# Optimization experiments

Hardware: AMD Instinct MI355X
Metric: run time of the kernel (lower is better)

The kernel has to match this reference:

```python
import jax, jax.numpy as jnp
import numpy as np

# Config constants (repo-level globals)
N, S, P = 4096, 64, 64          # total peds, scenes, peds per scene (uniform)
H, E, MLPD, BOT = 64, 16, 64, 32  # h_dim, EMBEDDING_DIM, MLP_DIM, BOTTLENECK_DIM
PRED_LEN = 12
MIN_DIM = 3                      # mlp_input_dim = [rel_pos(2), speed(1)]
PP_HID = 512                     # hidden width of mlp_pre_pool


def setup_inputs() -> dict:
    key = jax.random.key(0)
    ks = jax.random.split(key, 24)
    sc = 0.1
    starts = jnp.arange(S, dtype=jnp.int32) * P
    inp = {
        "last_pos": jax.random.normal(ks[0], (N, 2), jnp.float32),
        "last_pos_rel": jax.random.normal(ks[1], (N, 2), jnp.float32),
        "h0": jax.random.normal(ks[2], (1, N, H), jnp.float32),
        "c0": jax.random.normal(ks[3], (1, N, H), jnp.float32),
        "pred_ped_speed": jax.random.uniform(ks[4], (PRED_LEN, N, 1), jnp.float32),
        # spatial_embedding: Linear(3, E)
        "W_sp": jax.random.normal(ks[5], (MIN_DIM, E)) * sc, "b_sp": jnp.zeros(E),
        # LSTM cell (torch gate order i,f,g,o)
        "W_ih": jax.random.normal(ks[6], (E, 4 * H)) * sc, "b_ih": jnp.zeros(4 * H),
        "W_hh": jax.random.normal(ks[7], (H, 4 * H)) * sc, "b_hh": jnp.zeros(4 * H),
        # hidden2pos: Linear(H, 2)
        "W_h2p": jax.random.normal(ks[8], (H, 2)) * sc, "b_h2p": jnp.zeros(2),
        # pooling pos_embedding: Linear(3, E)
        "W_pe": jax.random.normal(ks[9], (MIN_DIM, E)) * sc, "b_pe": jnp.zeros(E),
        # mlp_pre_pool: [E+H, 512, BOT], relu, no BN
        "W_pp1": jax.random.normal(ks[10], (E + H, PP_HID)) * sc, "b_pp1": jnp.zeros(PP_HID),
        "W_pp2": jax.random.normal(ks[11], (PP_HID, BOT)) * sc, "b_pp2": jnp.zeros(BOT),
        # decoder mlp: [H+BOT, MLPD, H], relu, no BN
        "W_m1": jax.random.normal(ks[12], (H + BOT, MLPD)) * sc, "b_m1": jnp.zeros(MLPD),
        "W_m2": jax.random.normal(ks[13], (MLPD, H)) * sc, "b_m2": jnp.zeros(H),
        "seq_start_end": jnp.stack([starts, starts + P], axis=1),
        "train_or_test": 0,
    }
    return inp


def reference(last_pos, last_pos_rel, h0, c0, pred_ped_speed,
              W_sp, b_sp, W_ih, b_ih, W_hh, b_hh, W_h2p, b_h2p,
              W_pe, b_pe, W_pp1, b_pp1, W_pp2, b_pp2,
              W_m1, b_m1, W_m2, b_m2, seq_start_end, train_or_test):
    relu = jax.nn.relu

    def lstm_cell(x, h, c):
        g = x @ W_ih + b_ih + h @ W_hh + b_hh
        i, f, gg, o = jnp.split(g, 4, axis=-1)
        c = jax.nn.sigmoid(f) * c + jax.nn.sigmoid(i) * jnp.tanh(gg)
        h = jax.nn.sigmoid(o) * jnp.tanh(c)
        return h, c

    def pool(h, pos, spd):
        # uniform scenes: reshape [N,*] -> [S,P,*]; pairwise index [s,i,j]
        hg = h.reshape(S, P, H)
        pg = pos.reshape(S, P, 2)
        sg = spd.reshape(S, P, 1)
        # social feature [s,i,j] = pos[j] - pos[i]  (curr_end_pos_1 - curr_end_pos_2)
        rel = pg[:, None, :, :] - pg[:, :, None, :]              # [S,P,P,2]
        feat = jnp.concatenate(
            [rel, jnp.broadcast_to(sg[:, None, :, :], (S, P, P, 1))], -1)  # speed of j
        emb = feat @ W_pe + b_pe                                  # [S,P,P,E]
        pre = jnp.concatenate(
            [jnp.broadcast_to(hg[:, None, :, :], (S, P, P, H)), emb], -1)  # h of j
        x = relu(pre @ W_pp1 + b_pp1)
        x = relu(x @ W_pp2 + b_pp2)                               # [S,P,P,BOT]
        return x.max(axis=2).reshape(-1, BOT)                     # max over j -> [N,BOT]

    # speed used at step id is pred_ped_speed[id+1], last step reuses final speed
    spd_seq = jnp.concatenate([pred_ped_speed[1:], pred_ped_speed[-1:]], axis=0)
    x0 = jnp.concatenate([last_pos_rel, pred_ped_speed[0]], -1) @ W_sp + b_sp

    def step(carry, spd_t):
        h, c, lp, x = carry
        h, c = lstm_cell(x, h, c)
        rel_pos = h @ W_h2p + b_h2p
        curr = rel_pos + lp
        x_new = jnp.concatenate([rel_pos, spd_t], -1) @ W_sp + b_sp
        pool_h = pool(h, curr, spd_t)
        h_new = relu(relu(jnp.concatenate([h, pool_h], -1) @ W_m1 + b_m1) @ W_m2 + b_m2)
        return (h_new, c, curr, x_new), rel_pos

    carry = (h0[0], c0[0], last_pos, x0)
    _, rels = jax.lax.scan(step, carry, spd_seq)
    return rels  # [PRED_LEN, N, 2]
```

## Files before the change

kernel.cpp:

```cpp
#include <hip/hip_runtime.h>

typedef unsigned int  u32;
typedef unsigned short u16;
typedef float  f32x4 __attribute__((ext_vector_type(4)));
typedef u32    u32x4 __attribute__((ext_vector_type(4)));
typedef __bf16 bf16x8 __attribute__((ext_vector_type(8)));
typedef _Float16 f16;
typedef _Float16 f16x8 __attribute__((ext_vector_type(8)));
typedef _Float16 f16x2 __attribute__((ext_vector_type(2)));

static constexpr int NPED = 4096;
static constexpr int H = 64, E = 16, BOT = 32, PPH = 512;
static constexpr int TSTEPS = 12;

__device__ __forceinline__ float bf2f(u16 u) {
  return __builtin_bit_cast(float, ((u32)u) << 16);
}
__device__ __forceinline__ u16 f2bf(float f) {
  u32 u = __builtin_bit_cast(u32, f);
  u += 0x7fffu + ((u >> 16) & 1u);
  return (u16)(u >> 16);
}
__device__ __forceinline__ u16 f2h(float f) {
  return __builtin_bit_cast(u16, (f16)f);
}
__device__ __forceinline__ float sigm(float x) { return 1.f / (1.f + __expf(-x)); }
__device__ __forceinline__ float tanhf_(float x) {
  float t = fabsf(x);
  float e = __expf(-2.f * t);
  float r = (1.f - e) / (1.f + e);
  return x < 0.f ? -r : r;
}
__device__ __forceinline__ f16x8 relu8(f16x8 t) {
  const f16x8 z = {(f16)0, (f16)0, (f16)0, (f16)0, (f16)0, (f16)0, (f16)0, (f16)0};
#if __has_builtin(__builtin_elementwise_max)
  return __builtin_elementwise_max(t, z);
#else
  #pragma unroll
  for (int q = 0; q < 8; ++q) t[q] = t[q] > (f16)0 ? t[q] : (f16)0;
  return t;
#endif
}

static constexpr size_t OFF_C    = 0;
static constexpr size_t OFF_HL   = 1048576;
static constexpr size_t OFF_POS  = 2097152;
static constexpr size_t OFF_X    = 2129920;
static constexpr size_t OFF_POOL = 2392064;
static constexpr size_t OFF_ABF  = 2916352;
static constexpr size_t OFF_A3   = 7110656;
static constexpr size_t OFF_CST  = 7116800;
static constexpr size_t OFF_W2T  = 7118848;
static constexpr size_t OFF_GWH  = 7151616;
static constexpr size_t OFF_GWL  = 7200768;
static constexpr size_t OFF_D1H  = 7249920;
static constexpr size_t OFF_D1L  = 7262208;
static constexpr size_t OFF_D2H  = 7274496;
static constexpr size_t OFF_D2L  = 7282688;
static constexpr size_t OFF_PWH  = 7290880;
static constexpr size_t OFF_PWL  = 7356416;
static constexpr size_t OFF_ABF2 = 7421952;
static constexpr size_t ABF_BYTES = (size_t)NPED * PPH * 2;
static constexpr size_t WS_NEED_FUSED = OFF_ABF2 + ABF_BYTES;

static constexpr int POOL_SMEM = 64*520*2 + 32*520*2 + 16*512*2 + 16*4*2*16*4;
static constexpr int FUSED_SMEM = POOL_SMEM + 64 + 128 + 128;

__global__ void k_setup(const float* __restrict__ last_pos, const float* __restrict__ last_pos_rel,
                        const float* __restrict__ c0, const float* __restrict__ pps,
                        const float* __restrict__ W_sp, const float* __restrict__ b_sp,
                        const float* __restrict__ W_pe, const float* __restrict__ b_pe,
                        const float* __restrict__ W_pp1, const float* __restrict__ b_pp1,
                        const float* __restrict__ W_pp2,
                        const float* __restrict__ W_ih, const float* __restrict__ W_hh,
                        const float* __restrict__ W_m1, const float* __restrict__ W_m2,
                        float* __restrict__ c, float* __restrict__ pos, float* __restrict__ x,
                        float* __restrict__ A3, float* __restrict__ Cst, u16* __restrict__ W2t,
                        u16* GWH, u16* GWL, u16* D1H, u16* D1L,
                        u16* D2H, u16* D2L, u16* PWH, u16* PWL)
{
  const int stride = gridDim.x * blockDim.x;
  const int tid0 = blockIdx.x * blockDim.x + threadIdx.x;
  for (int i = tid0; i < NPED * H; i += stride) c[i] = c0[i];
  for (int i = tid0; i < NPED * 2; i += stride) pos[i] = last_pos[i];
  for (int i = tid0; i < NPED * E; i += stride) {
    int n = i >> 4, e = i & 15;
    x[i] = last_pos_rel[2*n] * W_sp[e] + last_pos_rel[2*n+1] * W_sp[16+e]
         + pps[n] * W_sp[32+e] + b_sp[e];
  }
  for (int i = tid0; i < 3 * PPH; i += stride) {
    int r = i >> 9, k = i & 511;
    float s = 0.f;
    for (int e = 0; e < 16; ++e) s += W_pe[r*16+e] * W_pp1[(64+e)*PPH + k];
    A3[i] = s;
  }
  for (int i = tid0; i < PPH; i += stride) {
    float s = b_pp1[i];
    for (int e = 0; e < 16; ++e) s += b_pe[e] * W_pp1[(64+e)*PPH + i];
    Cst[i] = s;
  }
  for (int i = tid0; i < 32 * PPH; i += stride) {
    int n = i >> 9, k = i & 511;
    W2t[i] = f2h(W_pp2[k*32 + n]);
  }
  for (int i = tid0; i < 256*96; i += stride) {
    int n = i / 96, k = i - n*96;
    float wv = (k < 16) ? W_ih[k*256+n] : ((k < 80) ? W_hh[(k-16)*256+n] : 0.f);
    u16 hi = f2bf(wv); u16 lo = f2bf(wv - bf2f(hi));
    int idx = (((n>>4)*3 + (k>>5))*64 + ((k>>3)&3)*16 + (n&15))*8 + (k&7);
    GWH[idx] = hi; GWL[idx] = lo;
  }
  for (int i = tid0; i < 64*96; i += stride) {
    int n = i / 96, k = i - n*96;
    float wv = W_m1[k*64 + n];
    u16 hi = f2bf(wv); u16 lo = f2bf(wv - bf2f(hi));
    int idx = (((n>>4)*3 + (k>>5))*64 + ((k>>3)&3)*16 + (n&15))*8 + (k&7);
    D1H[idx] = hi; D1L[idx] = lo;
  }
  for (int i = tid0; i < 64*64; i += stride) {
    int n = i >> 6, k = i & 63;
    float wv = W_m2[k*64 + n];
    u16 hi = f2bf(wv); u16 lo = f2bf(wv - bf2f(hi));
    int idx = (((n>>4)*2 + (k>>5))*64 + ((k>>3)&3)*16 + (n&15))*8 + (k&7);
    D2H[idx] = hi; D2L[idx] = lo;
  }
  for (int i = tid0; i < 512*64; i += stride) {
    int n = i >> 6, k = i & 63;
    float wv = W_pp1[k*PPH + n];
    u16 hi = f2bf(wv); u16 lo = f2bf(wv - bf2f(hi));
    int idx = (((n>>4)*2 + (k>>5))*64 + ((k>>3)&3)*16 + (n&15))*8 + (k&7);
    PWH[idx] = hi; PWL[idx] = lo;
  }
}

template<int NT, int NKS>
__device__ __forceinline__ void load_frags(const u16* __restrict__ WH, const u16* __restrict__ WL,
                                           int tile0, int lane,
                                           u32x4 (&bh)[NT][NKS], u32x4 (&bl)[NT][NKS])
{
  #pragma unroll
  for (int i = 0; i < NT; ++i)
    #pragma unroll
    for (int ks = 0; ks < NKS; ++ks) {
      int o = (((tile0 + i)*NKS + ks)*64 + lane)*8;
      bh[i][ks] = *(const u32x4*)(WH + o);
      bl[i][ks] = *(const u32x4*)(WL + o);
    }
}

template<int NT, int NKS>
__device__ __forceinline__ void mfma_compute(const u32x4 (&bh)[NT][NKS], const u32x4 (&bl)[NT][NKS],
                                             int lane, const float* arow, f32x4* acc)
{
  const int kg = lane >> 4;
  #pragma unroll
  for (int ks = 0; ks < NKS; ++ks) {
    f32x4 a0 = *(const f32x4*)(arow + ks*32 + kg*8);
    f32x4 a1 = *(const f32x4*)(arow + ks*32 + kg*8 + 4);
    float av[8] = {a0.x,a0.y,a0.z,a0.w,a1.x,a1.y,a1.z,a1.w};
    bf16x8 ah, al;
    #pragma unroll
    for (int j = 0; j < 8; ++j) {
      __bf16 hbits = (__bf16)av[j];
      ah[j] = hbits;
      al[j] = (__bf16)(av[j] - (float)hbits);
    }
    #pragma unroll
    for (int i = 0; i < NT; ++i) {
      bf16x8 BH = __builtin_bit_cast(bf16x8, bh[i][ks]);
      bf16x8 BL = __builtin_bit_cast(bf16x8, bl[i][ks]);
      acc[i] = __builtin_amdgcn_mfma_f32_16x16x32_bf16(ah, BH, acc[i], 0, 0, 0);
      acc[i] = __builtin_amdgcn_mfma_f32_16x16x32_bf16(ah, BL, acc[i], 0, 0, 0);
      acc[i] = __builtin_amdgcn_mfma_f32_16x16x32_bf16(al, BH, acc[i], 0, 0, 0);
    }
  }
}

template<int NT, int NKS>
__device__ __forceinline__ void mfma_block(
    const u16* __restrict__ WH, const u16* __restrict__ WL, int tile0, int lane,
    const float* arow, int acol0, f32x4* acc)
{
  u32x4 bh[NT][NKS], bl[NT][NKS];
  load_frags<NT,NKS>(WH, WL, tile0, lane, bh, bl);
  mfma_compute<NT,NKS>(bh, bl, lane, arow + acol0, acc);
}

__global__ __launch_bounds__(256) void k_step(
    int t,
    const float* __restrict__ h0, const float* __restrict__ pps,
    float* __restrict__ c, float* __restrict__ h_lstm,
    float* __restrict__ pos, float* __restrict__ x, const float* __restrict__ pool,
    const float* __restrict__ b_ih, const float* __restrict__ b_hh,
    const float* __restrict__ W_h2p, const float* __restrict__ b_h2p,
    const float* __restrict__ W_sp, const float* __restrict__ b_sp,
    const float* __restrict__ b_m1, const float* __restrict__ b_m2,
    const float* __restrict__ A3, const float* __restrict__ Cst,
    const u16* __restrict__ GWH, const u16* __restrict__ GWL,
    const u16* __restrict__ D1H, const u16* __restrict__ D1L,
    const u16* __restrict__ D2H, const u16* __restrict__ D2L,
    const u16* __restrict__ PWH, const u16* __restrict__ PWL,
    u16* __restrict__ a_bf, float* __restrict__ out)
{
  __shared__ float zin[16][100];
  __shared__ float o1[16][68];
  __shared__ float as_[16][100];
  __shared__ float hl[16][68];
  __shared__ float gl[16][260];
  __shared__ float rel_s[16][2], pos_s[16][2], spd_s[16];

  const int tid = threadIdx.x;
  const int p0 = blockIdx.x * 16;
  const int w = tid >> 6, lane = tid & 63, colq = lane & 15, kg = lane >> 4;
  const int tsp = (t + 1 < 12) ? t + 1 : 11;

  { int p = tid >> 4, e = tid & 15;
    as_[p][e] = x[(p0 + p) * E + e];
    as_[p][80 + e] = 0.f; }
  if (tid < 16) spd_s[tid] = pps[tsp * NPED + p0 + tid];
  if (t == 0) {
    #pragma unroll
    for (int q = 0; q < 4; ++q) {
      int idx = tid + 256*q; int p = idx >> 6, d = idx & 63;
      as_[p][16 + d] = h0[(p0 + p) * H + d];
    }
  } else {
    #pragma unroll
    for (int q = 0; q < 4; ++q) {
      int idx = tid + 256*q; int p = idx >> 6, d = idx & 63;
      zin[p][d] = h_lstm[(p0 + p) * H + d];
    }
    #pragma unroll
    for (int q = 0; q < 2; ++q) {
      int idx = tid + 256*q; int p = idx >> 5, d = idx & 31;
      zin[p][64 + d] = pool[(p0 + p) * BOT + d];
    }
  }
  __syncthreads();

  if (t > 0) {
    {
      f32x4 acc = {0.f, 0.f, 0.f, 0.f};
      mfma_block<1,3>(D1H, D1L, w, lane, &zin[colq][0], 0, &acc);
      int n = w*16 + colq;
      float bm = b_m1[n];
      #pragma unroll
      for (int r = 0; r < 4; ++r) o1[kg*4 + r][n] = fmaxf(acc[r] + bm, 0.f);
    }
    __syncthreads();
    {
      f32x4 acc = {0.f, 0.f, 0.f, 0.f};
      mfma_block<1,2>(D2H, D2L, w, lane, &o1[colq][0], 0, &acc);
      int n = w*16 + colq;
      float bm = b_m2[n];
      #pragma unroll
      for (int r = 0; r < 4; ++r) as_[kg*4 + r][16 + n] = fmaxf(acc[r] + bm, 0.f);
    }
    __syncthreads();
  }

  {
    f32x4 gacc[4];
    #pragma unroll
    for (int i = 0; i < 4; ++i) gacc[i] = (f32x4){0.f,0.f,0.f,0.f};
    mfma_block<2,3>(GWH, GWL, w*4,     lane, &as_[colq][0], 0, &gacc[0]);
    mfma_block<2,3>(GWH, GWL, w*4 + 2, lane, &as_[colq][0], 0, &gacc[2]);
    #pragma unroll
    for (int i = 0; i < 4; ++i) {
      int n = (w*4 + i)*16 + colq;
      float bb = b_ih[n] + b_hh[n];
      #pragma unroll
      for (int r = 0; r < 4; ++r) gl[kg*4 + r][n] = gacc[i][r] + bb;
    }
  }
  __syncthreads();

  #pragma unroll
  for (int q = 0; q < 4; ++q) {
    int idx = tid + 256*q; int p = idx >> 6, d = idx & 63; int n = p0 + p;
    float gi = gl[p][d], gf = gl[p][64 + d], gg = gl[p][128 + d], go = gl[p][192 + d];
    float cv = c[n*H + d];
    float cn = sigm(gf) * cv + sigm(gi) * tanhf_(gg);
    float hv = sigm(go) * tanhf_(cn);
    c[n*H + d] = cn;
    hl[p][d] = hv;
    h_lstm[n*H + d] = hv;
  }
  __syncthreads();

  {
    int p = tid >> 4, l = tid & 15;
    f32x4 hv = *(const f32x4*)(&hl[p][0] + l*4);
    float s0 = hv.x * W_h2p[(l*4+0)*2]   + hv.y * W_h2p[(l*4+1)*2]
             + hv.z * W_h2p[(l*4+2)*2]   + hv.w * W_h2p[(l*4+3)*2];
    float s1 = hv.x * W_h2p[(l*4+0)*2+1] + hv.y * W_h2p[(l*4+1)*2+1]
             + hv.z * W_h2p[(l*4+2)*2+1] + hv.w * W_h2p[(l*4+3)*2+1];
    #pragma unroll
    for (int m = 1; m < 16; m <<= 1) {
      s0 += __shfl_xor(s0, m, 64);
      s1 += __shfl_xor(s1, m, 64);
    }
    if (l == 0) {
      float r0 = s0 + b_h2p[0], r1 = s1 + b_h2p[1];
      int n = p0 + p;
      float px = pos[n*2] + r0, py = pos[n*2+1] + r1;
      pos[n*2] = px; pos[n*2+1] = py;
      rel_s[p][0] = r0; rel_s[p][1] = r1;
      pos_s[p][0] = px; pos_s[p][1] = py;
      out[(t*NPED + n)*2] = r0; out[(t*NPED + n)*2 + 1] = r1;
    }
  }
  __syncthreads();

  if (t < 11) {
    {
      int p = tid >> 4, e = tid & 15;
      float xv = rel_s[p][0] * W_sp[e] + rel_s[p][1] * W_sp[16+e]
               + spd_s[p] * W_sp[32+e] + b_sp[e];
      x[(p0 + p) * E + e] = xv;
    }
    {
      f32x4 pacc[8];
      #pragma unroll
      for (int i = 0; i < 8; ++i) pacc[i] = (f32x4){0.f,0.f,0.f,0.f};
      mfma_block<4,2>(PWH, PWL, w*8,     lane, &hl[colq][0], 0, &pacc[0]);
      mfma_block<4,2>(PWH, PWL, w*8 + 4, lane, &hl[colq][0], 0, &pacc[4]);
      #pragma unroll
      for (int i = 0; i < 8; ++i) {
        int n = (w*8 + i)*16 + colq;
        float a3x = A3[n], a3y = A3[512 + n], a3s = A3[1024 + n], cst = Cst[n];
        #pragma unroll
        for (int r = 0; r < 4; ++r) {
          int p2 = kg*4 + r;
          float val = pacc[i][r] + pos_s[p2][0]*a3x + pos_s[p2][1]*a3y
                    + spd_s[p2]*a3s + cst;
          a_bf[(size_t)(p0 + p2)*PPH + n] = f2h(val);
        }
      }
    }
  }
}

__global__ __launch_bounds__(1024) void k_pool(
    const u16* __restrict__ a_bf, const float* __restrict__ pos,
    const float* __restrict__ A3, const u16* __restrict__ W2t,
    const float* __restrict__ b_pp2, float* __restrict__ pool)
{
  constexpr int LDA = 520;
  extern __shared__ char smem_raw[];
  u16* a_s  = (u16*)smem_raw;
  u16* w2_s = a_s + 64 * LDA;
  f16* v_s  = (f16*)(w2_s + 32 * LDA);
  float* red = (float*)(v_s + 16 * 512);

  const int tid = threadIdx.x;
  const int s = blockIdx.y;
  const int i0 = blockIdx.x * 16;

  for (int idx = tid; idx < 4096; idx += 1024) {
    int r = idx >> 6, c8 = (idx & 63) * 8;
    *(u32x4*)&a_s[r * LDA + c8] = *(const u32x4*)&a_bf[(s * 64 + r) * PPH + c8];
  }
  for (int idx = tid; idx < 2048; idx += 1024) {
    int r = idx >> 6, c8 = (idx & 63) * 8;
    *(u32x4*)&w2_s[r * LDA + c8] = *(const u32x4*)&W2t[r * PPH + c8];
  }
  for (int idx = tid; idx < 4096; idx += 1024) {
    int i = idx >> 8, k2 = (idx & 255) * 2;
    int n = s * 64 + i0 + i;
    float px = pos[n * 2], py = pos[n * 2 + 1];
    float v0 = px * A3[k2]     + py * A3[512 + k2];
    float v1 = px * A3[k2 + 1] + py * A3[512 + k2 + 1];
    f16x2 pk = { (f16)v0, (f16)v1 };
    *(f16x2*)&v_s[i * 512 + k2] = pk;
  }
  __syncthreads();

  const int lane = tid & 63, w = tid >> 6;
  const int jq = w & 3, g = w >> 2;
  const int col = lane & 15, kg = lane >> 4;
  const int aoff  = (jq * 16 + col) * LDA + kg * 8;
  const int w0off = col * LDA + kg * 8;
  const int w1off = (col + 16) * LDA + kg * 8;
  const float b20 = b_pp2[col];
  const float b21 = b_pp2[col + 16];
  const f32x4 vzero = {0.f, 0.f, 0.f, 0.f};

  f32x4 accA[4], accB[4];
  #pragma unroll
  for (int ii = 0; ii < 4; ++ii) { accA[ii] = vzero; accB[ii] = vzero; }

  for (int kk = 0; kk < 16; ++kk) {
    const int ke = kk * 32;
    f16x8 a8  = __builtin_bit_cast(f16x8, *(const u32x4*)&a_s[aoff + ke]);
    f16x8 bw0 = __builtin_bit_cast(f16x8, *(const u32x4*)&w2_s[w0off + ke]);
    f16x8 bw1 = __builtin_bit_cast(f16x8, *(const u32x4*)&w2_s[w1off + ke]);
    #pragma unroll
    for (int ii = 0; ii < 4; ++ii) {
      f16x8 v8 = *(const f16x8*)&v_s[(g * 4 + ii) * 512 + ke + kg * 8];
      f16x8 tq = relu8(a8 - v8);
      accA[ii] = __builtin_amdgcn_mfma_f32_16x16x32_f16(tq, bw0, accA[ii], 0, 0, 0);
      accB[ii] = __builtin_amdgcn_mfma_f32_16x16x32_f16(tq, bw1, accB[ii], 0, 0, 0);
    }
  }

  #pragma unroll
  for (int ii = 0; ii < 4; ++ii) {
    float m0 = 0.f, m1 = 0.f;
    #pragma unroll
    for (int r = 0; r < 4; ++r) {
      m0 = fmaxf(m0, accA[ii][r] + b20);
      m1 = fmaxf(m1, accB[ii][r] + b21);
    }
    m0 = fmaxf(m0, __shfl_xor(m0, 16, 64));
    m0 = fmaxf(m0, __shfl_xor(m0, 32, 64));
    m1 = fmaxf(m1, __shfl_xor(m1, 16, 64));
    m1 = fmaxf(m1, __shfl_xor(m1, 32, 64));
    if (kg == 0) {
      red[((w * 4 + ii) * 2 + 0) * 16 + col] = m0;
      red[((w * 4 + ii) * 2 + 1) * 16 + col] = m1;
    }
  }
  __syncthreads();

  if (tid < 512) {
    int gg = tid >> 7, ii = (tid >> 5) & 3, tile = (tid >> 4) & 1, cc = tid & 15;
    float m = red[(((gg * 4 + 0) * 4 + ii) * 2 + tile) * 16 + cc];
    #pragma unroll
    for (int q = 1; q < 4; ++q)
      m = fmaxf(m, red[(((gg * 4 + q) * 4 + ii) * 2 + tile) * 16 + cc]);
    int i = i0 + gg * 4 + ii;
    pool[(s * 64 + i) * 32 + tile * 16 + cc] = m;
  }
}

__global__ __launch_bounds__(1024) void k_fused(
    int t,
    const float* __restrict__ pps,
    float* __restrict__ c, float* __restrict__ h_lstm,
    float* __restrict__ pos, float* __restrict__ x,
    const float* __restrict__ b_ih, const float* __restrict__ b_hh,
    const float* __restrict__ W_h2p, const float* __restrict__ b_h2p,
    const float* __restrict__ W_sp, const float* __restrict__ b_sp,
    const float* __restrict__ b_m1, const float* __restrict__ b_m2,
    const float* __restrict__ A3, const float* __restrict__ Cst,
    const u16* __restrict__ GWH, const u16* __restrict__ GWL,
    const u16* __restrict__ D1H, const u16* __restrict__ D1L,
    const u16* __restrict__ D2H, const u16* __restrict__ D2L,
    const u16* __restrict__ PWH, const u16* __restrict__ PWL,
    const u16* __restrict__ W2t, const float* __restrict__ b_pp2,
    const u16* __restrict__ a_read, u16* __restrict__ a_write,
    float* __restrict__ out)
{
  constexpr int LDA = 520;
  extern __shared__ char smem_raw[];
  u16*   a_s    = (u16*)smem_raw;
  u16*   w2_s   = a_s + 64 * LDA;
  f16*   v_s    = (f16*)(w2_s + 32 * LDA);
  float* red    = (float*)(v_s + 16 * 512);
  float* spd_s  = red + 16*4*2*16;
  float* rel_s  = spd_s + 16;
  float* pos_s  = rel_s + 32;
  float* zin = (float*)smem_raw;
  float* o1  = zin + 16*100;
  float* as_ = o1  + 16*68;
  float* hl  = as_ + 16*100;
  float* gl  = hl  + 16*68;

  const int tid = threadIdx.x;
  const int s = blockIdx.y;
  const int i0 = blockIdx.x * 16;
  const int p0 = s * 64 + i0;
  const int lane = tid & 63, w = tid >> 6;
  const int colq = lane & 15, kg = lane >> 4;
  const int sd = tid & 63;
  const int tsp = (t + 1 < 12) ? t + 1 : 11;

  float hreg = h_lstm[(p0 + w) * H + sd];
  float creg = c[(p0 + w) * H + sd];
  float whp0 = W_h2p[2 * sd], whp1 = W_h2p[2 * sd + 1];
  float xreg = 0.f;
  if (tid < 256) xreg = x[(p0 + (tid >> 4)) * E + (tid & 15)];
  if (tid < 16) spd_s[tid] = pps[tsp * NPED + p0 + tid];

  for (int idx = tid; idx < 4096; idx += 1024) {
    int r = idx >> 6, c8 = (idx & 63) * 8;
    *(u32x4*)&a_s[r * LDA + c8] = *(const u32x4*)&a_read[(s * 64 + r) * PPH + c8];
  }
  for (int idx = tid; idx < 2048; idx += 1024) {
    int r = idx >> 6, c8 = (idx & 63) * 8;
    *(u32x4*)&w2_s[r * LDA + c8] = *(const u32x4*)&W2t[r * PPH + c8];
  }
  for (int idx = tid; idx < 4096; idx += 1024) {
    int i = idx >> 8, k2 = (idx & 255) * 2;
    int n = s * 64 + i0 + i;
    float px = pos[n * 2], py = pos[n * 2 + 1];
    float v0 = px * A3[k2]     + py * A3[512 + k2];
    float v1 = px * A3[k2 + 1] + py * A3[512 + k2 + 1];
    f16x2 pk = { (f16)v0, (f16)v1 };
    *(f16x2*)&v_s[i * 512 + k2] = pk;
  }
  __syncthreads();

  u32x4 gh[1][3], glo[1][3];
  u32x4 d1h_[1][3], d1l_[1][3], d2h_[1][2], d2l_[1][2];

  {
    const int jq = w & 3, g = w >> 2;
    const int aoff  = (jq * 16 + colq) * LDA + kg * 8;
    const int w0off = colq * LDA + kg * 8;
    const int w1off = (colq + 16) * LDA + kg * 8;
    const float b20 = b_pp2[colq];
    const float b21 = b_pp2[colq + 16];
    const f32x4 vzero = {0.f, 0.f, 0.f, 0.f};

    f32x4 accA[4], accB[4];
    #pragma unroll
    for (int ii = 0; ii < 4; ++ii) { accA[ii] = vzero; accB[ii] = vzero; }

    for (int kk = 0; kk < 16; ++kk) {
      const int ke = kk * 32;
      f16x8 a8  = __builtin_bit_cast(f16x8, *(const u32x4*)&a_s[aoff + ke]);
      f16x8 bw0 = __builtin_bit_cast(f16x8, *(const u32x4*)&w2_s[w0off + ke]);
      f16x8 bw1 = __builtin_bit_cast(f16x8, *(const u32x4*)&w2_s[w1off + ke]);
      #pragma unroll
      for (int ii = 0; ii < 4; ++ii) {
        f16x8 v8 = *(const f16x8*)&v_s[(g * 4 + ii) * 512 + ke + kg * 8];
        f16x8 tq = relu8(a8 - v8);
        accA[ii] = __builtin_amdgcn_mfma_f32_16x16x32_f16(tq, bw0, accA[ii], 0, 0, 0);
        accB[ii] = __builtin_amdgcn_mfma_f32_16x16x32_f16(tq, bw1, accB[ii], 0, 0, 0);
      }
    }

    #pragma unroll
    for (int ii = 0; ii < 4; ++ii) {
      float m0 = 0.f, m1 = 0.f;
      #pragma unroll
      for (int r = 0; r < 4; ++r) {
        m0 = fmaxf(m0, accA[ii][r] + b20);
        m1 = fmaxf(m1, accB[ii][r] + b21);
      }
      m0 = fmaxf(m0, __shfl_xor(m0, 16, 64));
      m0 = fmaxf(m0, __shfl_xor(m0, 32, 64));
      m1 = fmaxf(m1, __shfl_xor(m1, 16, 64));
      m1 = fmaxf(m1, __shfl_xor(m1, 32, 64));
      if (kg == 0) {
        red[((w * 4 + ii) * 2 + 0) * 16 + colq] = m0;
        red[((w * 4 + ii) * 2 + 1) * 16 + colq] = m1;
      }
    }
  }
  load_frags<1,3>(GWH, GWL, w, lane, gh, glo);
  if (w < 4) {
    load_frags<1,3>(D1H, D1L, w, lane, d1h_, d1l_);
    load_frags<1,2>(D2H, D2L, w, lane, d2h_, d2l_);
  }
  __syncthreads();

  zin[w * 100 + sd] = hreg;
  if (tid < 512) {
    int gg = tid >> 7, ii = (tid >> 5) & 3, tile = (tid >> 4) & 1, cc = tid & 15;
    float m = red[(((gg * 4 + 0) * 4 + ii) * 2 + tile) * 16 + cc];
    #pragma unroll
    for (int q = 1; q < 4; ++q)
      m = fmaxf(m, red[(((gg * 4 + q) * 4 + ii) * 2 + tile) * 16 + cc]);
    zin[(gg * 4 + ii) * 100 + 64 + tile * 16 + cc] = m;
  }
  if (tid < 256) { int p = tid >> 4, e = tid & 15;
                   as_[p * 100 + e] = xreg; as_[p * 100 + 80 + e] = 0.f; }
  __syncthreads();

  if (w < 4) {
    f32x4 acc = {0.f, 0.f, 0.f, 0.f};
    mfma_compute<1,3>(d1h_, d1l_, lane, &zin[colq * 100], &acc);
    int n = w * 16 + colq;
    float bm = b_m1[n];
    #pragma unroll
    for (int r = 0; r < 4; ++r) o1[(kg * 4 + r) * 68 + n] = fmaxf(acc[r] + bm, 0.f);
  }
  __syncthreads();

  if (w < 4) {
    f32x4 acc = {0.f, 0.f, 0.f, 0.f};
    mfma_compute<1,2>(d2h_, d2l_, lane, &o1[colq * 68], &acc);
    int n = w * 16 + colq;
    float bm = b_m2[n];
    #pragma unroll
    for (int r = 0; r < 4; ++r) as_[(kg * 4 + r) * 100 + 16 + n] = fmaxf(acc[r] + bm, 0.f);
  }
  __syncthreads();

  {
    f32x4 acc = {0.f, 0.f, 0.f, 0.f};
    mfma_compute<1,3>(gh, glo, lane, &as_[colq * 100], &acc);
    int n = w * 16 + colq;
    float bb = b_ih[n] + b_hh[n];
    #pragma unroll
    for (int r = 0; r < 4; ++r) gl[(kg * 4 + r) * 260 + n] = acc[r] + bb;
  }
  u32x4 ph[2][2], pl[2][2];
  if (t < 11) load_frags<2,2>(PWH, PWL, w * 2, lane, ph, pl);
  __syncthreads();

  {
    int n = p0 + w;
    float gi = gl[w*260 + sd], gf = gl[w*260 + 64 + sd],
          gg = gl[w*260 + 128 + sd], go = gl[w*260 + 192 + sd];
    float cn = sigm(gf) * creg + sigm(gi) * tanhf_(gg);
    float hv = sigm(go) * tanhf_(cn);
    c[n*H + sd] = cn;
    hl[w*68 + sd] = hv;
    h_lstm[n*H + sd] = hv;
    float s0 = hv * whp0, s1 = hv * whp1;
    #pragma unroll
    for (int m = 1; m < 64; m <<= 1) {
      s0 += __shfl_xor(s0, m, 64);
      s1 += __shfl_xor(s1, m, 64);
    }
    if (sd == 0) {
      float r0 = s0 + b_h2p[0], r1 = s1 + b_h2p[1];
      float px = pos[n*2] + r0, py = pos[n*2+1] + r1;
      pos[n*2] = px; pos[n*2+1] = py;
      rel_s[w*2+0] = r0; rel_s[w*2+1] = r1;
      pos_s[w*2+0] = px; pos_s[w*2+1] = py;
      out[(t*NPED + n)*2] = r0; out[(t*NPED + n)*2 + 1] = r1;
    }
  }
  __syncthreads();

  if (t < 11) {
    if (tid < 256) {
      int p = tid >> 4, e = tid & 15;
      float xv = rel_s[p*2+0] * W_sp[e] + rel_s[p*2+1] * W_sp[16+e]
               + spd_s[p] * W_sp[32+e] + b_sp[e];
      x[(p0 + p) * E + e] = xv;
    }
    {
      f32x4 pacc[2];
      pacc[0] = (f32x4){0.f,0.f,0.f,0.f};
      pacc[1] = (f32x4){0.f,0.f,0.f,0.f};
      mfma_compute<2,2>(ph, pl, lane, &hl[colq * 68], pacc);
      #pragma unroll
      for (int i = 0; i < 2; ++i) {
        int n = (w * 2 + i) * 16 + colq;
        float a3x = A3[n], a3y = A3[512 + n], a3s = A3[1024 + n], cst = Cst[n];
        #pragma unroll
        for (int r = 0; r < 4; ++r) {
          int p2 = kg * 4 + r;
          float val = pacc[i][r] + pos_s[p2*2+0]*a3x + pos_s[p2*2+1]*a3y
                    + spd_s[p2]*a3s + cst;
          a_write[(size_t)(p0 + p2) * PPH + n] = f2h(val);
        }
      }
    }
  }
}

extern "C" void kernel_launch(void* const* d_in, const int* in_sizes, int n_in,
                              void* d_out, int out_size, void* d_ws, size_t ws_size,
                              hipStream_t stream)
{
  const float* last_pos     = (const float*)d_in[0];
  const float* last_pos_rel = (const float*)d_in[1];
  const float* h0    = (const float*)d_in[2];
  const float* c0    = (const float*)d_in[3];
  const float* pps   = (const float*)d_in[4];
  const float* W_sp  = (const float*)d_in[5];
  const float* b_sp  = (const float*)d_in[6];
  const float* W_ih  = (const float*)d_in[7];
  const float* b_ih  = (const float*)d_in[8];
  const float* W_hh  = (const float*)d_in[9];
  const float* b_hh  = (const float*)d_in[10];
  const float* W_h2p = (const float*)d_in[11];
  const float* b_h2p = (const float*)d_in[12];
  const float* W_pe  = (const float*)d_in[13];
  const float* b_pe  = (const float*)d_in[14];
  const float* W_pp1 = (const float*)d_in[15];
  const float* b_pp1 = (const float*)d_in[16];
  const float* W_pp2 = (const float*)d_in[17];
  const float* b_pp2 = (const float*)d_in[18];
  const float* W_m1  = (const float*)d_in[19];
  const float* b_m1  = (const float*)d_in[20];
  const float* W_m2  = (const float*)d_in[21];
  const float* b_m2  = (const float*)d_in[22];

  char* ws = (char*)d_ws;
  float* c_buf  = (float*)(ws + OFF_C);
  float* h_lstm = (float*)(ws + OFF_HL);
  float* pos    = (float*)(ws + OFF_POS);
  float* x_buf  = (float*)(ws + OFF_X);
  float* pool   = (float*)(ws + OFF_POOL);
  u16*   abuf0  = (u16*)(ws + OFF_ABF);
  float* A3     = (float*)(ws + OFF_A3);
  float* Cst    = (float*)(ws + OFF_CST);
  u16*   W2t    = (u16*)(ws + OFF_W2T);
  u16* GWH = (u16*)(ws + OFF_GWH); u16* GWL = (u16*)(ws + OFF_GWL);
  u16* D1H = (u16*)(ws + OFF_D1H); u16* D1L = (u16*)(ws + OFF_D1L);
  u16* D2H = (u16*)(ws + OFF_D2H); u16* D2L = (u16*)(ws + OFF_D2L);
  u16* PWH = (u16*)(ws + OFF_PWH); u16* PWL = (u16*)(ws + OFF_PWL);
  u16*   abuf1  = (u16*)(ws + OFF_ABF2);
  float* out    = (float*)d_out;

  const bool fused_ok = (ws_size >= WS_NEED_FUSED);

  hipFuncSetAttribute(reinterpret_cast<const void*>(k_pool),
                      hipFuncAttributeMaxDynamicSharedMemorySize, POOL_SMEM);
  hipFuncSetAttribute(reinterpret_cast<const void*>(k_fused),
                      hipFuncAttributeMaxDynamicSharedMemorySize, FUSED_SMEM);

  k_setup<<<512, 256, 0, stream>>>(last_pos, last_pos_rel, c0, pps, W_sp, b_sp,
                                   W_pe, b_pe, W_pp1, b_pp1, W_pp2,
                                   W_ih, W_hh, W_m1, W_m2,
                                   c_buf, pos, x_buf, A3, Cst, W2t,
                                   GWH, GWL, D1H, D1L, D2H, D2L, PWH, PWL);

  k_step<<<256, 256, 0, stream>>>(0, h0, pps, c_buf, h_lstm, pos, x_buf, pool,
                                  b_ih, b_hh, W_h2p, b_h2p, W_sp, b_sp,
                                  b_m1, b_m2, A3, Cst,
                                  GWH, GWL, D1H, D1L, D2H, D2L, PWH, PWL,
                                  abuf0, out);

  if (fused_ok) {
    for (int t = 1; t < TSTEPS; ++t) {
      const u16* ar = ((t - 1) & 1) ? abuf1 : abuf0;
      u16*       aw = (t & 1)       ? abuf1 : abuf0;
      k_fused<<<dim3(4, 64), 1024, FUSED_SMEM, stream>>>(
          t, pps, c_buf, h_lstm, pos, x_buf,
          b_ih, b_hh, W_h2p, b_h2p, W_sp, b_sp, b_m1, b_m2, A3, Cst,
          GWH, GWL, D1H, D1L, D2H, D2L, PWH, PWL,
          W2t, b_pp2, ar, aw, out);
    }
  } else {
    for (int t = 1; t < TSTEPS; ++t) {
      k_pool<<<dim3(4, 64), 1024, POOL_SMEM, stream>>>(abuf0, pos, A3, W2t, b_pp2, pool);
      k_step<<<256, 256, 0, stream>>>(t, h0, pps, c_buf, h_lstm, pos, x_buf, pool,
                                      b_ih, b_hh, W_h2p, b_h2p, W_sp, b_sp,
                                      b_m1, b_m2, A3, Cst,
                                      GWH, GWL, D1H, D1L, D2H, D2L, PWH, PWL,
                                      abuf0, out);
    }
  }
}
```

Measured before the change: 276.7 us.

## Run step 0 in fused kernel and stage pool tiles via global_load_lds

Step 0 now runs through the fused 1024-thread kernel with a short path that skips pooling and the decoder MLP, and reads h from h0. This replaces the separate k_step launch and its different grid. The A and W2t tiles are copied into LDS with direct global-to-LDS loads instead of passing through registers, which is meant to cut VGPR traffic and load latency. The change adds a t==0 branch and depends on the global_load_lds builtin being available and on its per-lane LDS addressing being correct.

```diff
diff --git a/kernel.cpp b/kernel.cpp
--- a/kernel.cpp
+++ b/kernel.cpp
@@ -39,6 +39,16 @@
   #pragma unroll
   for (int q = 0; q < 8; ++q) t[q] = t[q] > (f16)0 ? t[q] : (f16)0;
   return t;
+#endif
+}
+
+__device__ __forceinline__ void gload_lds16(const u16* __restrict__ g, u16* l) {
+#if __has_builtin(__builtin_amdgcn_global_load_lds)
+  __builtin_amdgcn_global_load_lds(
+      (const __attribute__((address_space(1))) void*)g,
+      (__attribute__((address_space(3))) void*)l, 16, 0, 0);
+#else
+  *(u32x4*)l = *(const u32x4*)g;
 #endif
 }
 
@@ -436,7 +446,7 @@
 
 __global__ __launch_bounds__(1024) void k_fused(
     int t,
-    const float* __restrict__ pps,
+    const float* __restrict__ h0, const float* __restrict__ pps,
     float* __restrict__ c, float* __restrict__ h_lstm,
     float* __restrict__ pos, float* __restrict__ x,
     const float* __restrict__ b_ih, const float* __restrict__ b_hh,
@@ -476,119 +486,132 @@
   const int sd = tid & 63;
   const int tsp = (t + 1 < 12) ? t + 1 : 11;
 
-  float hreg = h_lstm[(p0 + w) * H + sd];
+  const float* hsrc = (t == 0) ? h0 : h_lstm;
+  float hreg = hsrc[(p0 + w) * H + sd];
   float creg = c[(p0 + w) * H + sd];
   float whp0 = W_h2p[2 * sd], whp1 = W_h2p[2 * sd + 1];
   float xreg = 0.f;
   if (tid < 256) xreg = x[(p0 + (tid >> 4)) * E + (tid & 15)];
   if (tid < 16) spd_s[tid] = pps[tsp * NPED + p0 + tid];
 
-  for (int idx = tid; idx < 4096; idx += 1024) {
-    int r = idx >> 6, c8 = (idx & 63) * 8;
-    *(u32x4*)&a_s[r * LDA + c8] = *(const u32x4*)&a_read[(s * 64 + r) * PPH + c8];
-  }
-  for (int idx = tid; idx < 2048; idx += 1024) {
-    int r = idx >> 6, c8 = (idx & 63) * 8;
-    *(u32x4*)&w2_s[r * LDA + c8] = *(const u32x4*)&W2t[r * PPH + c8];
-  }
-  for (int idx = tid; idx < 4096; idx += 1024) {
-    int i = idx >> 8, k2 = (idx & 255) * 2;
-    int n = s * 64 + i0 + i;
-    float px = pos[n * 2], py = pos[n * 2 + 1];
-    float v0 = px * A3[k2]     + py * A3[512 + k2];
-    float v1 = px * A3[k2 + 1] + py * A3[512 + k2 + 1];
-    f16x2 pk = { (f16)v0, (f16)v1 };
-    *(f16x2*)&v_s[i * 512 + k2] = pk;
-  }
-  __syncthreads();
-
   u32x4 gh[1][3], glo[1][3];
   u32x4 d1h_[1][3], d1l_[1][3], d2h_[1][2], d2l_[1][2];
 
-  {
-    const int jq = w & 3, g = w >> 2;
-    const int aoff  = (jq * 16 + colq) * LDA + kg * 8;
-    const int w0off = colq * LDA + kg * 8;
-    const int w1off = (colq + 16) * LDA + kg * 8;
-    const float b20 = b_pp2[colq];
-    const float b21 = b_pp2[colq + 16];
-    const f32x4 vzero = {0.f, 0.f, 0.f, 0.f};
-
-    f32x4 accA[4], accB[4];
-    #pragma unroll
-    for (int ii = 0; ii < 4; ++ii) { accA[ii] = vzero; accB[ii] = vzero; }
-
-    for (int kk = 0; kk < 16; ++kk) {
-      const int ke = kk * 32;
-      f16x8 a8  = __builtin_bit_cast(f16x8, *(const u32x4*)&a_s[aoff + ke]);
-      f16x8 bw0 = __builtin_bit_cast(f16x8, *(const u32x4*)&w2_s[w0off + ke]);
-      f16x8 bw1 = __builtin_bit_cast(f16x8, *(const u32x4*)&w2_s[w1off + ke]);
+  if (t > 0) {
+    #pragma unroll
+    for (int q = 0; q < 4; ++q) {
+      int r = w + 16 * q;
+      gload_lds16(&a_read[(size_t)(s * 64 + r) * PPH + lane * 8],
+                  &a_s[r * LDA + lane * 8]);
+    }
+    #pragma unroll
+    for (int q = 0; q < 2; ++q) {
+      int r = w + 16 * q;
+      gload_lds16(&W2t[(size_t)r * PPH + lane * 8],
+                  &w2_s[r * LDA + lane * 8]);
+    }
+    for (int idx = tid; idx < 4096; idx += 1024) {
+      int i = idx >> 8, k2 = (idx & 255) * 2;
+      int n = s * 64 + i0 + i;
+      float px = pos[n * 2], py = pos[n * 2 + 1];
+      float v0 = px * A3[k2]     + py * A3[512 + k2];
+      float v1 = px * A3[k2 + 1] + py * A3[512 + k2 + 1];
+      f16x2 pk = { (f16)v0, (f16)v1 };
+      *(f16x2*)&v_s[i * 512 + k2] = pk;
+    }
+    __syncthreads();
+
+    {
+      const int jq = w & 3, g = w >> 2;
+      const int aoff  = (jq * 16 + colq) * LDA + kg * 8;
+      const int w0off = colq * LDA + kg * 8;
+      const int w1off = (colq + 16) * LDA + kg * 8;
+      const float b20 = b_pp2[colq];
+      const float b21 = b_pp2[colq + 16];
+      const f32x4 vzero = {0.f, 0.f, 0.f, 0.f};
+
+      f32x4 accA[4], accB[4];
+      #pragma unroll
+      for (int ii = 0; ii < 4; ++ii) { accA[ii] = vzero; accB[ii] = vzero; }
+
+      for (int kk = 0; kk < 16; ++kk) {
+        const int ke = kk * 32;
+        f16x8 a8  = __builtin_bit_cast(f16x8, *(const u32x4*)&a_s[aoff + ke]);
+        f16x8 bw0 = __builtin_bit_cast(f16x8, *(const u32x4*)&w2_s[w0off + ke]);
+        f16x8 bw1 = __builtin_bit_cast(f16x8, *(const u32x4*)&w2_s[w1off + ke]);
+        #pragma unroll
+        for (int ii = 0; ii < 4; ++ii) {
+          f16x8 v8 = *(const f16x8*)&v_s[(g * 4 + ii) * 512 + ke + kg * 8];
+          f16x8 tq = relu8(a8 - v8);
+          accA[ii] = __builtin_amdgcn_mfma_f32_16x16x32_f16(tq, bw0, accA[ii], 0, 0, 0);
+          accB[ii] = __builtin_amdgcn_mfma_f32_16x16x32_f16(tq, bw1, accB[ii], 0, 0, 0);
+        }
+      }
+
       #pragma unroll
       for (int ii = 0; ii < 4; ++ii) {
-        f16x8 v8 = *(const f16x8*)&v_s[(g * 4 + ii) * 512 + ke + kg * 8];
-        f16x8 tq = relu8(a8 - v8);
-        accA[ii] = __builtin_amdgcn_mfma_f32_16x16x32_f16(tq, bw0, accA[ii], 0, 0, 0);
-        accB[ii] = __builtin_amdgcn_mfma_f32_16x16x32_f16(tq, bw1, accB[ii], 0, 0, 0);
+        float m0 = 0.f, m1 = 0.f;
+        #pragma unroll
+        for (int r = 0; r < 4; ++r) {
+          m0 = fmaxf(m0, accA[ii][r] + b20);
+          m1 = fmaxf(m1, accB[ii][r] + b21);
+        }
+        m0 = fmaxf(m0, __shfl_xor(m0, 16, 64));
+        m0 = fmaxf(m0, __shfl_xor(m0, 32, 64));
+        m1 = fmaxf(m1, __shfl_xor(m1, 16, 64));
+        m1 = fmaxf(m1, __shfl_xor(m1, 32, 64));
+        if (kg == 0) {
+          red[((w * 4 + ii) * 2 + 0) * 16 + colq] = m0;
+          red[((w * 4 + ii) * 2 + 1) * 16 + colq] = m1;
+        }
       }
     }
-
-    #pragma unroll
-    for (int ii = 0; ii < 4; ++ii) {
-      float m0 = 0.f, m1 = 0.f;
-      #pragma unroll
-      for (int r = 0; r < 4; ++r) {
-        m0 = fmaxf(m0, accA[ii][r] + b20);
-        m1 = fmaxf(m1, accB[ii][r] + b21);
-      }
-      m0 = fmaxf(m0, __shfl_xor(m0, 16, 64));
-      m0 = fmaxf(m0, __shfl_xor(m0, 32, 64));
-      m1 = fmaxf(m1, __shfl_xor(m1, 16, 64));
-      m1 = fmaxf(m1, __shfl_xor(m1, 32, 64));
-      if (kg == 0) {
-        red[((w * 4 + ii) * 2 + 0) * 16 + colq] = m0;
-        red[((w * 4 + ii) * 2 + 1) * 16 + colq] = m1;
-      }
-    }
-  }
-  load_frags<1,3>(GWH, GWL, w, lane, gh, glo);
-  if (w < 4) {
-    load_frags<1,3>(D1H, D1L, w, lane, d1h_, d1l_);
-    load_frags<1,2>(D2H, D2L, w, lane, d2h_, d2l_);
-  }
-  __syncthreads();
-
-  zin[w * 100 + sd] = hreg;
-  if (tid < 512) {
-    int gg = tid >> 7, ii = (tid >> 5) & 3, tile = (tid >> 4) & 1, cc = tid & 15;
-    float m = red[(((gg * 4 + 0) * 4 + ii) * 2 + tile) * 16 + cc];
-    #pragma unroll
-    for (int q = 1; q < 4; ++q)
-      m = fmaxf(m, red[(((gg * 4 + q) * 4 + ii) * 2 + tile) * 16 + cc]);
-    zin[(gg * 4 + ii) * 100 + 64 + tile * 16 + cc] = m;
-  }
-  if (tid < 256) { int p = tid >> 4, e = tid & 15;
-                   as_[p * 100 + e] = xreg; as_[p * 100 + 80 + e] = 0.f; }
-  __syncthreads();
-
-  if (w < 4) {
-    f32x4 acc = {0.f, 0.f, 0.f, 0.f};
-    mfma_compute<1,3>(d1h_, d1l_, lane, &zin[colq * 100], &acc);
-    int n = w * 16 + colq;
-    float bm = b_m1[n];
-    #pragma unroll
-    for (int r = 0; r < 4; ++r) o1[(kg * 4 + r) * 68 + n] = fmaxf(acc[r] + bm, 0.f);
-  }
-  __syncthreads();
-
-  if (w < 4) {
-    f32x4 acc = {0.f, 0.f, 0.f, 0.f};
-    mfma_compute<1,2>(d2h_, d2l_, lane, &o1[colq * 68], &acc);
-    int n = w * 16 + colq;
-    float bm = b_m2[n];
-    #pragma unroll
-    for (int r = 0; r < 4; ++r) as_[(kg * 4 + r) * 100 + 16 + n] = fmaxf(acc[r] + bm, 0.f);
-  }
-  __syncthreads();
+    load_frags<1,3>(GWH, GWL, w, lane, gh, glo);
+    if (w < 4) {
+      load_frags<1,3>(D1H, D1L, w, lane, d1h_, d1l_);
+      load_frags<1,2>(D2H, D2L, w, lane, d2h_, d2l_);
+    }
+    __syncthreads();
+
+    zin[w * 100 + sd] = hreg;
+    if (tid < 512) {
+      int gg = tid >> 7, ii = (tid >> 5) & 3, tile = (tid >> 4) & 1, cc = tid & 15;
+      float m = red[(((gg * 4 + 0) * 4 + ii) * 2 + tile) * 16 + cc];
+      #pragma unroll
+      for (int q = 1; q < 4; ++q)
+        m = fmaxf(m, red[(((gg * 4 + q) * 4 + ii) * 2 + tile) * 16 + cc]);
+      zin[(gg * 4 + ii) * 100 + 64 + tile * 16 + cc] = m;
+    }
+    if (tid < 256) { int p = tid >> 4, e = tid & 15;
+                     as_[p * 100 + e] = xreg; as_[p * 100 + 80 + e] = 0.f; }
+    __syncthreads();
+
+    if (w < 4) {
+      f32x4 acc = {0.f, 0.f, 0.f, 0.f};
+      mfma_compute<1,3>(d1h_, d1l_, lane, &zin[colq * 100], &acc);
+      int n = w * 16 + colq;
+      float bm = b_m1[n];
+      #pragma unroll
+      for (int r = 0; r < 4; ++r) o1[(kg * 4 + r) * 68 + n] = fmaxf(acc[r] + bm, 0.f);
+    }
+    __syncthreads();
+
+    if (w < 4) {
+      f32x4 acc = {0.f, 0.f, 0.f, 0.f};
+      mfma_compute<1,2>(d2h_, d2l_, lane, &o1[colq * 68], &acc);
+      int n = w * 16 + colq;
+      float bm = b_m2[n];
+      #pragma unroll
+      for (int r = 0; r < 4; ++r) as_[(kg * 4 + r) * 100 + 16 + n] = fmaxf(acc[r] + bm, 0.f);
+    }
+    __syncthreads();
+  } else {
+    load_frags<1,3>(GWH, GWL, w, lane, gh, glo);
+    as_[w * 100 + 16 + sd] = hreg;
+    if (tid < 256) { int p = tid >> 4, e = tid & 15;
+                     as_[p * 100 + e] = xreg; as_[p * 100 + 80 + e] = 0.f; }
+    __syncthreads();
+  }
 
   {
     f32x4 acc = {0.f, 0.f, 0.f, 0.f};
@@ -714,23 +737,22 @@
                                    c_buf, pos, x_buf, A3, Cst, W2t,
                                    GWH, GWL, D1H, D1L, D2H, D2L, PWH, PWL);
 
-  k_step<<<256, 256, 0, stream>>>(0, h0, pps, c_buf, h_lstm, pos, x_buf, pool,
-                                  b_ih, b_hh, W_h2p, b_h2p, W_sp, b_sp,
-                                  b_m1, b_m2, A3, Cst,
-                                  GWH, GWL, D1H, D1L, D2H, D2L, PWH, PWL,
-                                  abuf0, out);
-
   if (fused_ok) {
-    for (int t = 1; t < TSTEPS; ++t) {
-      const u16* ar = ((t - 1) & 1) ? abuf1 : abuf0;
-      u16*       aw = (t & 1)       ? abuf1 : abuf0;
+    for (int t = 0; t < TSTEPS; ++t) {
+      const u16* ar = (t > 0 && ((t - 1) & 1)) ? abuf1 : abuf0;
+      u16*       aw = (t & 1) ? abuf1 : abuf0;
       k_fused<<<dim3(4, 64), 1024, FUSED_SMEM, stream>>>(
-          t, pps, c_buf, h_lstm, pos, x_buf,
+          t, h0, pps, c_buf, h_lstm, pos, x_buf,
           b_ih, b_hh, W_h2p, b_h2p, W_sp, b_sp, b_m1, b_m2, A3, Cst,
           GWH, GWL, D1H, D1L, D2H, D2L, PWH, PWL,
           W2t, b_pp2, ar, aw, out);
     }
   } else {
+    k_step<<<256, 256, 0, stream>>>(0, h0, pps, c_buf, h_lstm, pos, x_buf, pool,
+                                    b_ih, b_hh, W_h2p, b_h2p, W_sp, b_sp,
+                                    b_m1, b_m2, A3, Cst,
+                                    GWH, GWL, D1H, D1L, D2H, D2L, PWH, PWL,
+                                    abuf0, out);
     for (int t = 1; t < TSTEPS; ++t) {
       k_pool<<<dim3(4, 64), 1024, POOL_SMEM, stream>>>(abuf0, pos, A3, W2t, b_pp2, pool);
       k_step<<<256, 256, 0, stream>>>(t, h0, pps, c_buf, h_lstm, pos, x_buf, pool,
```

Result: faster. 266.6 us, median of 2 (-3.7%).
